# Kernel tuning notes

Hardware: AMD Instinct MI355X
Metric: run time of the kernel (lower is better)

Reference implementation:

```python
import jax, jax.numpy as jnp
import numpy as np

TARGET_MAIN_CONTRIBUTION = 0.6
CONTRIB_LOSS_COEF = 0.01
TOP_K = 2
NEG_INF = -1e9


def _gat(x, adj, W1, a1s, a1d, W2, a2s, a2d):
    """Dense 2-layer GAT (pyGAT style): multi-head concat + ELU, then one output head.
    x: [B,S,Fin], adj: [B,S,S], W1: [H,Fin,Fh], a1s/a1d: [H,Fh], W2: [H*Fh,Fout], a2s/a2d: [Fout]."""
    mask = adj > 0  # [B,S,S]
    h = jnp.einsum('bsf,hfo->bhso', x, W1)                      # [B,H,S,Fh]
    es = jnp.einsum('bhso,ho->bhs', h, a1s)
    ed = jnp.einsum('bhso,ho->bhs', h, a1d)
    e = jax.nn.leaky_relu(es[:, :, :, None] + ed[:, :, None, :], 0.2)  # [B,H,S,S]
    att = jax.nn.softmax(jnp.where(mask[:, None], e, NEG_INF), axis=-1)
    h1 = jax.nn.elu(jnp.einsum('bhst,bhto->bhso', att, h))      # [B,H,S,Fh]
    B, H, S, Fh = h1.shape
    h1 = h1.transpose(0, 2, 1, 3).reshape(B, S, H * Fh)         # concat heads
    h2 = h1 @ W2                                                # [B,S,Fout]
    e2 = jax.nn.leaky_relu((h2 @ a2s)[:, :, None] + (h2 @ a2d)[:, None, :], 0.2)
    att2 = jax.nn.softmax(jnp.where(mask, e2, NEG_INF), axis=-1)
    return jnp.einsum('bst,bto->bso', att2, h2)


def setup_inputs() -> dict:
    B, S, D, H, Hd, E = 4, 1024, 256, 6, 64, 3
    key = jax.random.key(0)
    ks = jax.random.split(key, 20)
    feature = jax.random.normal(ks[0], (B, S, D), dtype=jnp.float32)
    # sparse-ish binary adjacency with self-loops
    adj = (jax.random.uniform(ks[1], (B, S, S)) < 0.05).astype(jnp.float32)
    adj = jnp.maximum(adj, jnp.eye(S, dtype=jnp.float32)[None])
    p = lambda k, shape: jax.random.normal(k, shape, dtype=jnp.float32) * 0.1
    return {
        'feature': feature, 'adj': adj,
        'main_W1': p(ks[2], (H, D, Hd)), 'main_a1s': p(ks[3], (H, Hd)), 'main_a1d': p(ks[4], (H, Hd)),
        'main_W2': p(ks[5], (H * Hd, D)), 'main_a2s': p(ks[6], (D,)), 'main_a2d': p(ks[7], (D,)),
        'dep_W1': p(ks[8], (E, H, D, Hd)), 'dep_a1s': p(ks[9], (E, H, Hd)), 'dep_a1d': p(ks[10], (E, H, Hd)),
        'dep_W2': p(ks[11], (E, H * Hd, D)), 'dep_a2s': p(ks[12], (E, D)), 'dep_a2d': p(ks[13], (E, D)),
        'router_W': p(ks[14], (D, E)),
        'blend_W': p(ks[15], (D, D)), 'blend_b': jnp.zeros((D,), dtype=jnp.float32),
        'doc_num': 4, 'sect_num': 32,
    }


def reference(feature, adj, main_W1, main_a1s, main_a1d, main_W2, main_a2s, main_a2d,
              dep_W1, dep_a1s, dep_a1d, dep_W2, dep_a2s, dep_a2d,
              router_W, blend_W, blend_b, doc_num, sect_num):
    B, S, D = feature.shape
    E = router_W.shape[1]
    # main expert on full graph
    main_output = _gat(feature, adj, main_W1, main_a1s, main_a1d, main_W2, main_a2s, main_a2d)
    # per-expert adjacency views (zero out columns by node type)
    col = jnp.arange(S)
    sent_cols = (col < S - sect_num - doc_num).astype(adj.dtype)
    sect_cols = ((col >= S - sect_num - doc_num) & (col < S - doc_num)).astype(adj.dtype)
    doc_cols = (col >= S - doc_num).astype(adj.dtype)
    adj_stack = jnp.stack([adj * sent_cols, adj * sect_cols, adj * doc_cols])  # [E,B,S,S]
    # fixed top-k router
    x_flat = feature.reshape(-1, D)
    gate_probs = jax.nn.softmax(x_flat @ router_W, axis=-1)      # [B*S,E]
    _, top_idx = jax.lax.top_k(gate_probs, TOP_K)                # [B*S,k]
    routing_mask = jax.nn.one_hot(top_idx, E, dtype=feature.dtype).sum(axis=-2)  # [B*S,E] binary
    routing_mask = routing_mask.reshape(B, S, E)
    mask_e = routing_mask.transpose(2, 0, 1)[..., None]          # [E,B,S,1]
    # deputy experts: masked input, masked output, accumulate
    x_e = feature[None] * mask_e                                 # [E,B,S,D]
    dep_out = jax.vmap(_gat)(x_e, adj_stack, dep_W1, dep_a1s, dep_a1d, dep_W2, dep_a2s, dep_a2d)
    deputy_output = (dep_out * mask_e).sum(axis=0)               # [B,S,D]
    # blend gate
    blend_weight = jax.nn.sigmoid(feature @ blend_W + blend_b)
    final_output = blend_weight * main_output + (1.0 - blend_weight) * deputy_output
    main_contribution = blend_weight.mean()
    contribution_loss = jnp.abs(main_contribution - TARGET_MAIN_CONTRIBUTION) * CONTRIB_LOSS_COEF
    return final_output, contribution_loss, main_contribution
```

## Files before the change

### kernel.cpp

```cpp
#include <hip/hip_runtime.h>
#include <math.h>

#define B 4
#define S 1024
#define D 256
#define H 6
#define HD 64
#define NE 3
#define HHD 384
#define ROWS (B*S)
#define MAXN 128

typedef __attribute__((ext_vector_type(8))) short bf8_t;
typedef __attribute__((ext_vector_type(4))) float f32x4;

__device__ __forceinline__ float leaky(float x){ return x > 0.f ? x : 0.2f*x; }

__device__ __forceinline__ unsigned short f2bf(float f){
    union { float f; unsigned int u; } v; v.f = f;
    unsigned int u = v.u;
    return (unsigned short)((u + 0x7FFFu + ((u >> 16) & 1u)) >> 16);
}
__device__ __forceinline__ float bf2f(unsigned short h){
    union { unsigned int u; float f; } v; v.u = ((unsigned int)h) << 16;
    return v.f;
}
__device__ __forceinline__ float blo(unsigned int u){
    union { unsigned int u; float f; } v; v.u = u << 16; return v.f;
}
__device__ __forceinline__ float bhi(unsigned int u){
    union { unsigned int u; float f; } v; v.u = u & 0xffff0000u; return v.f;
}
__device__ __forceinline__ float i2f(int t){
    union { int i; float f; } v; v.i = t; return v.f;
}
__device__ __forceinline__ int f2i(float f){
    union { float f; int i; } v; v.f = f; return v.i;
}

#define PB_CONV   1024
#define PB_NBR    1024
#define PB_W1     1536
#define PB_W2     1536
#define PB_BW      256
#define PB_ZERO    177
#define PB_ROUTER 1024
#define PB_TOTAL  (PB_CONV + PB_NBR + PB_W1 + PB_W2 + PB_BW + PB_ZERO + PB_ROUTER)
#define NZERO     45088

__global__ __launch_bounds__(256) void prep_misc_kernel(
        const float* __restrict__ feature, const float* __restrict__ adj,
        const float* __restrict__ main_W1, const float* __restrict__ dep_W1,
        const float* __restrict__ main_W2, const float* __restrict__ dep_W2,
        const float* __restrict__ blend_W, const float* __restrict__ router_W,
        const int* __restrict__ doc_p, const int* __restrict__ sect_p,
        unsigned short* __restrict__ featbf, short* __restrict__ nbr,
        int4* __restrict__ nbc, unsigned short* __restrict__ w1nk,
        unsigned short* __restrict__ w2nk, unsigned short* __restrict__ bwt,
        float* __restrict__ zbase, float* __restrict__ rmask)
{
    int blk = blockIdx.x, tid = threadIdx.x;
    if (blk < PB_CONV){
        int idx = blk*256 + tid;
        float4 v = ((const float4*)feature)[idx];
        ushort4 o;
        o.x = f2bf(v.x); o.y = f2bf(v.y); o.z = f2bf(v.z); o.w = f2bf(v.w);
        ((ushort4*)featbf)[idx] = o;
        return;
    }
    blk -= PB_CONV;
    if (blk < PB_NBR){
        int wave = tid >> 6, lane = tid & 63;
        int row = blk*4 + wave;
        int b1 = S - *sect_p - *doc_p;
        int b2 = S - *doc_p;
        const float* ar = adj + (size_t)row*S + lane*16;
        float a[16];
        #pragma unroll
        for (int q = 0; q < 4; q++){
            float4 v = ((const float4*)ar)[q];
            a[q*4+0] = v.x; a[q*4+1] = v.y; a[q*4+2] = v.z; a[q*4+3] = v.w;
        }
        int t0 = lane*16;
        int k = 0, c1 = 0, c2 = 0;
        #pragma unroll
        for (int i = 0; i < 16; i++){
            if (a[i] > 0.f){
                k++;
                int t = t0 + i;
                if (t < b1) c1++;
                if (t < b2) c2++;
            }
        }
        int inc = k;
        #pragma unroll
        for (int d = 1; d < 64; d <<= 1){
            int u = __shfl_up(inc, d);
            if (lane >= d) inc += u;
        }
        int off = inc - k;
        int total = __shfl(inc, 63);
        int o = row*MAXN + off;
        #pragma unroll
        for (int i = 0; i < 16; i++){
            if (a[i] > 0.f) nbr[o++] = (short)(t0 + i);
        }
        for (int d = 32; d; d >>= 1){
            c1 += __shfl_down(c1, d);
            c2 += __shfl_down(c2, d);
        }
        if (lane == 0) nbc[row] = make_int4(total, c1, c2, 0);
        return;
    }
    blk -= PB_NBR;
    if (blk < PB_W1){
        int e = blk / 384;
        int idx = (blk - e*384)*256 + tid;
        const float* src = (e == 0) ? main_W1 : dep_W1 + (size_t)(e-1)*H*D*HD;
        int n = idx >> 8, k = idx & 255;
        int h = n >> 6, o = n & 63;
        w1nk[(size_t)e*HHD*D + idx] = f2bf(src[(h*D + k)*HD + o]);
        return;
    }
    blk -= PB_W1;
    if (blk < PB_W2){
        int g = blk*256 + tid;
        int e = g / (D*HHD);
        int rem = g - e*(D*HHD);
        int n = rem / HHD, k = rem - n*HHD;
        const float* src = (e == 0) ? main_W2 : dep_W2 + (size_t)(e-1)*HHD*D;
        w2nk[g] = f2bf(src[k*D + n]);
        return;
    }
    blk -= PB_W2;
    if (blk < PB_BW){
        int col = blk, k = tid;
        bwt[col*D + k] = f2bf(blend_W[k*D + col]);
        return;
    }
    blk -= PB_BW;
    if (blk < PB_ZERO){
        int idx = blk*256 + tid;
        if (idx < NZERO) zbase[idx] = 0.f;
        return;
    }
    blk -= PB_ZERO;
    {
        int wave = tid >> 6, lane = tid & 63;
        int row = blk*4 + wave;
        float4 xv = ((const float4*)(feature + (size_t)row*D))[lane];
        int f = lane*4;
        float xa[4] = {xv.x, xv.y, xv.z, xv.w};
        float p0 = 0.f, p1 = 0.f, p2 = 0.f;
        #pragma unroll
        for (int j = 0; j < 4; j++){
            p0 += xa[j]*router_W[(f+j)*NE + 0];
            p1 += xa[j]*router_W[(f+j)*NE + 1];
            p2 += xa[j]*router_W[(f+j)*NE + 2];
        }
        for (int off = 32; off; off >>= 1){
            p0 += __shfl_down(p0, off);
            p1 += __shfl_down(p1, off);
            p2 += __shfl_down(p2, off);
        }
        if (lane == 0){
            float p[3] = {p0, p1, p2};
            int ex = 0;
            for (int e = 1; e < NE; e++) if (p[e] <= p[ex]) ex = e;
            for (int e = 0; e < NE; e++) rmask[e*ROWS + row] = (e == ex) ? 0.f : 1.f;
        }
    }
}

__global__ __launch_bounds__(256, 4) void gemm1_kernel(const unsigned short* __restrict__ w1nk,
                                                    const unsigned short* __restrict__ featbf,
                                                    const float* __restrict__ rmask,
                                                    const float* __restrict__ main_a1s,
                                                    const float* __restrict__ main_a1d,
                                                    const float* __restrict__ dep_a1s,
                                                    const float* __restrict__ dep_a1d,
                                                    const unsigned short* __restrict__ bwt,
                                                    const float* __restrict__ bb,
                                                    unsigned short* __restrict__ htn4,
                                                    float* __restrict__ es8,
                                                    float* __restrict__ ed8,
                                                    float* __restrict__ meanV1p,
                                                    float* __restrict__ gatebuf,
                                                    float* __restrict__ sumBuf){
    __shared__ float ep[2][2][64][17];
    int tid = threadIdx.x, wave = tid >> 6, lane = tid & 63;
    int quad = lane >> 4, l16 = lane & 15;
    int e = blockIdx.z;
    int n0 = blockIdx.y*64;
    f32x4 z4 = {0.f,0.f,0.f,0.f};
    bf8_t bz = {0,0,0,0,0,0,0,0};

    if (e == 4){
        if (blockIdx.x >= 2) return;
        int m0 = blockIdx.x*128;
        const unsigned short* arow0 = bwt + (size_t)(m0 + wave*16 + l16)*D + quad*8;
        const unsigned short* arow1 = arow0 + (size_t)64*D;
        const unsigned short* brow[4];
        #pragma unroll
        for (int j = 0; j < 4; j++)
            brow[j] = featbf + (size_t)(n0 + j*16 + l16)*D + quad*8;
        f32x4 acc[8] = {z4, z4, z4, z4, z4, z4, z4, z4};
        bf8_t a0F = *(const bf8_t*)(arow0);
        bf8_t a1F = *(const bf8_t*)(arow1);
        bf8_t bF[4];
        #pragma unroll
        for (int j = 0; j < 4; j++) bF[j] = *(const bf8_t*)(brow[j]);
        #pragma unroll
        for (int it = 0; it < D/32; it++){
            bf8_t a0C = a0F, a1C = a1F;
            bf8_t bC[4] = {bF[0], bF[1], bF[2], bF[3]};
            if (it + 1 < D/32){
                int kn = (it + 1)*32;
                a0F = *(const bf8_t*)(arow0 + kn);
                a1F = *(const bf8_t*)(arow1 + kn);
                #pragma unroll
                for (int j = 0; j < 4; j++) bF[j] = *(const bf8_t*)(brow[j] + kn);
            }
            #pragma unroll
            for (int j = 0; j < 4; j++){
                acc[j]   = __builtin_amdgcn_mfma_f32_16x16x32_bf16(a0C, bC[j], acc[j],   0, 0, 0);
                acc[4+j] = __builtin_amdgcn_mfma_f32_16x16x32_bf16(a1C, bC[j], acc[4+j], 0, 0, 0);
            }
        }
        int mbase0 = m0 + wave*16 + quad*4;
        int mbase1 = mbase0 + 64;
        float bias0[4], bias1[4];
        #pragma unroll
        for (int r = 0; r < 4; r++){ bias0[r] = bb[mbase0 + r]; bias1[r] = bb[mbase1 + r]; }
        float lsum = 0.f;
        #pragma unroll
        for (int j = 0; j < 4; j++){
            int rown = n0 + j*16 + l16;
            f32x4 st0, st1;
            #pragma unroll
            for (int r = 0; r < 4; r++){
                float g0 = 1.f/(1.f + __expf(-(acc[j][r] + bias0[r])));
                float g1 = 1.f/(1.f + __expf(-(acc[4+j][r] + bias1[r])));
                lsum += g0 + g1;
                st0[r] = g0; st1[r] = g1;
            }
            *(f32x4*)(gatebuf + (size_t)rown*D + mbase0) = st0;
            *(f32x4*)(gatebuf + (size_t)rown*D + mbase1) = st1;
        }
        float* redp = &ep[0][0][0][0];
        redp[tid] = lsum;
        __syncthreads();
        for (int sft = 128; sft; sft >>= 1){
            if (tid < sft) redp[tid] += redp[tid + sft];
            __syncthreads();
        }
        if (tid == 0) atomicAdd(sumBuf, redp[0]);
        return;
    }

    int p = blockIdx.x;
    int m0 = p*128;
    const unsigned short* arow0 = w1nk + (size_t)e*HHD*D + (size_t)(m0 + wave*16 + l16)*D + quad*8;
    const unsigned short* arow1 = arow0 + (size_t)64*D;
    const unsigned short* brow[4];
    bool zr[4];
    #pragma unroll
    for (int j = 0; j < 4; j++){
        int n = n0 + j*16 + l16;
        brow[j] = featbf + (size_t)n*D + quad*8;
        zr[j] = (e > 0) ? (rmask[(size_t)(e-1)*ROWS + n] == 0.f) : false;
    }
    f32x4 acc[8] = {z4, z4, z4, z4, z4, z4, z4, z4};
    bf8_t a0F = *(const bf8_t*)(arow0);
    bf8_t a1F = *(const bf8_t*)(arow1);
    bf8_t bF[4];
    #pragma unroll
    for (int j = 0; j < 4; j++) bF[j] = zr[j] ? bz : *(const bf8_t*)(brow[j]);
    #pragma unroll
    for (int it = 0; it < D/32; it++){
        bf8_t a0C = a0F, a1C = a1F;
        bf8_t bC[4] = {bF[0], bF[1], bF[2], bF[3]};
        if (it + 1 < D/32){
            int kn = (it + 1)*32;
            a0F = *(const bf8_t*)(arow0 + kn);
            a1F = *(const bf8_t*)(arow1 + kn);
            #pragma unroll
            for (int j = 0; j < 4; j++) bF[j] = zr[j] ? bz : *(const bf8_t*)(brow[j] + kn);
        }
        #pragma unroll
        for (int j = 0; j < 4; j++){
            acc[j]   = __builtin_amdgcn_mfma_f32_16x16x32_bf16(a0C, bC[j], acc[j],   0, 0, 0);
            acc[4+j] = __builtin_amdgcn_mfma_f32_16x16x32_bf16(a1C, bC[j], acc[4+j], 0, 0, 0);
        }
    }
    int b = n0 >> 10;
    int mbase0 = m0 + wave*16 + quad*4;
    int mbase1 = mbase0 + 64;
    int obase = wave*16 + quad*4;
    int h0 = p*2, h1 = p*2 + 1;
    #pragma unroll
    for (int j = 0; j < 4; j++){
        int row = n0 + j*16 + l16;
        ushort4 o0, o1;
        o0.x = f2bf(acc[j][0]);   o0.y = f2bf(acc[j][1]);
        o0.z = f2bf(acc[j][2]);   o0.w = f2bf(acc[j][3]);
        o1.x = f2bf(acc[4+j][0]); o1.y = f2bf(acc[4+j][1]);
        o1.z = f2bf(acc[4+j][2]); o1.w = f2bf(acc[4+j][3]);
        *(ushort4*)(htn4 + ((size_t)e*ROWS + row)*HHD + mbase0) = o0;
        *(ushort4*)(htn4 + ((size_t)e*ROWS + row)*HHD + mbase1) = o1;
    }
    const float* a1sp = (e == 0) ? main_a1s : dep_a1s + (size_t)(e-1)*H*HD;
    const float* a1dp = (e == 0) ? main_a1d : dep_a1d + (size_t)(e-1)*H*HD;
    float s0v[4], d0v[4], s1v[4], d1v[4];
    #pragma unroll
    for (int r = 0; r < 4; r++){
        s0v[r] = a1sp[mbase0 + r]; d0v[r] = a1dp[mbase0 + r];
        s1v[r] = a1sp[mbase1 + r]; d1v[r] = a1dp[mbase1 + r];
    }
    #pragma unroll
    for (int j = 0; j < 4; j++){
        float ps0 = 0.f, pd0 = 0.f, ps1 = 0.f, pd1 = 0.f;
        #pragma unroll
        for (int r = 0; r < 4; r++){
            ps0 += acc[j][r]*s0v[r];   pd0 += acc[j][r]*d0v[r];
            ps1 += acc[4+j][r]*s1v[r]; pd1 += acc[4+j][r]*d1v[r];
        }
        ep[0][0][j*16 + l16][wave*4 + quad] = ps0;
        ep[0][1][j*16 + l16][wave*4 + quad] = pd0;
        ep[1][0][j*16 + l16][wave*4 + quad] = ps1;
        ep[1][1][j*16 + l16][wave*4 + quad] = pd1;
    }
    float* mvb = meanV1p + ((size_t)e*B + b)*512;
    #pragma unroll
    for (int r = 0; r < 4; r++){
        float cm0 = acc[0][r] + acc[1][r] + acc[2][r] + acc[3][r];
        float cm1 = acc[4][r] + acc[5][r] + acc[6][r] + acc[7][r];
        for (int off = 8; off; off >>= 1){
            cm0 += __shfl_down(cm0, off, 16);
            cm1 += __shfl_down(cm1, off, 16);
        }
        if (l16 == 0){
            atomicAdd(mvb + (obase + r)*8 + h0, cm0*(1.f/(float)S));
            atomicAdd(mvb + (obase + r)*8 + h1, cm1*(1.f/(float)S));
        }
    }
    __syncthreads();
    {
        int hh = tid >> 7, arr = (tid >> 6) & 1, sl = tid & 63;
        float sum = 0.f;
        #pragma unroll
        for (int i = 0; i < 16; i++) sum += ep[hh][arr][sl][i];
        int n = n0 + sl;
        float* dst = arr ? ed8 : es8;
        dst[(((size_t)e*B + (n >> 10))*S + (n & 1023))*8 + (p*2 + hh)] = sum;
    }
}

__global__ __launch_bounds__(128) void attn1_gather_kernel(const unsigned short* __restrict__ htn4,
                                                           const float* __restrict__ es8,
                                                           const float* __restrict__ ed8,
                                                           const short* __restrict__ nbr,
                                                           const int4* __restrict__ nbc,
                                                           const float* __restrict__ meanV1p,
                                                           unsigned short* __restrict__ h1c4){
    __shared__ float wrec[MAXN][8];
    __shared__ float pacc[64][8];
    __shared__ float pden[2][8];
    int wave = threadIdx.x >> 6, lane = threadIdx.x & 63;
    int s = blockIdx.x;
    int e = blockIdx.y >> 2, b = blockIdx.y & 3;
    int row = b*S + s;
    int4 c = nbc[row];
    int lo = 0, hi = c.x;
    if (e == 1) hi = c.y;
    else if (e == 2){ lo = c.y; hi = c.z; }
    else if (e == 3){ lo = c.z; }
    int nn = hi - lo;
    const float* esp = es8 + (((size_t)e*B + b)*S + s)*8;
    f32x4 es_lo = *(const f32x4*)esp;
    f32x4 es_hi = *(const f32x4*)(esp + 4);
    float esv[6] = {es_lo[0], es_lo[1], es_lo[2], es_lo[3], es_hi[0], es_hi[1]};
    const float* edb = ed8 + ((size_t)e*B + b)*S*8;
    const short* nl = nbr + (size_t)row*MAXN;
    int i = wave*64 + lane;
    float w[6] = {0,0,0,0,0,0};
    if (i < nn){
        int t = nl[lo + i];
        const float* epn = edb + (size_t)t*8;
        f32x4 d0 = *(const f32x4*)epn;
        f32x4 d1 = *(const f32x4*)(epn + 4);
        float edv[6] = {d0[0], d0[1], d0[2], d0[3], d1[0], d1[1]};
        #pragma unroll
        for (int h = 0; h < 6; h++) w[h] = __expf(leaky(esv[h] + edv[h]));
        f32x4 r0 = {w[0], w[1], w[2], w[3]};
        f32x4 r1 = {w[4], w[5], i2f(t), 0.f};
        *(f32x4*)&wrec[i][0] = r0;
        *(f32x4*)&wrec[i][4] = r1;
    }
    #pragma unroll
    for (int h = 0; h < 6; h++){
        float x = w[h];
        for (int o2 = 32; o2; o2 >>= 1) x += __shfl_down(x, o2);
        if (lane == 0) pden[wave][h] = x;
    }
    __syncthreads();
    const unsigned short* Vb = htn4 + ((size_t)e*ROWS + b*S)*HHD + lane;
    float acc[6] = {0,0,0,0,0,0};
    #pragma unroll 4
    for (int j = wave; j < nn; j += 2){
        f32x4 r0 = *(const f32x4*)&wrec[j][0];
        f32x4 r1 = *(const f32x4*)&wrec[j][4];
        int t = f2i(r1[2]);
        const unsigned short* vp = Vb + (size_t)t*HHD;
        float v0 = bf2f(vp[0]);
        float v1 = bf2f(vp[64]);
        float v2 = bf2f(vp[128]);
        float v3 = bf2f(vp[192]);
        float v4 = bf2f(vp[256]);
        float v5 = bf2f(vp[320]);
        acc[0] += r0[0]*v0; acc[1] += r0[1]*v1;
        acc[2] += r0[2]*v2; acc[3] += r0[3]*v3;
        acc[4] += r1[0]*v4; acc[5] += r1[1]*v5;
    }
    if (wave == 1){
        f32x4 p0 = {acc[0], acc[1], acc[2], acc[3]};
        f32x4 p1 = {acc[4], acc[5], 0.f, 0.f};
        *(f32x4*)&pacc[lane][0] = p0;
        *(f32x4*)&pacc[lane][4] = p1;
    }
    __syncthreads();
    if (wave == 0){
        unsigned short* outp = h1c4 + ((size_t)e*ROWS + row)*HHD;
        const float* mv = meanV1p + ((size_t)e*B + b)*512 + lane*8;
        #pragma unroll
        for (int h = 0; h < 6; h++){
            float den = pden[0][h] + pden[1][h];
            float v = (nn > 0) ? (acc[h] + pacc[lane][h])/den : mv[h];
            v = v > 0.f ? v : __expf(v) - 1.f;
            outp[h*64 + lane] = f2bf(v);
        }
    }
}

__global__ __launch_bounds__(256, 4) void gemm2_kernel(const unsigned short* __restrict__ w2nk,
                                                    const unsigned short* __restrict__ h1c4,
                                                    const float* __restrict__ main_a2s,
                                                    const float* __restrict__ main_a2d,
                                                    const float* __restrict__ dep_a2s,
                                                    const float* __restrict__ dep_a2d,
                                                    unsigned short* __restrict__ h2n4,
                                                    float* __restrict__ f2s4,
                                                    float* __restrict__ f2d4,
                                                    float* __restrict__ meanV2){
    __shared__ float ep[2][2][64][17];
    int tid = threadIdx.x, wave = tid >> 6, lane = tid & 63;
    int quad = lane >> 4, l16 = lane & 15;
    int e = blockIdx.z;
    int m0 = blockIdx.x*128;
    int n0 = blockIdx.y*64;
    f32x4 z4 = {0.f,0.f,0.f,0.f};
    const unsigned short* arow0 = w2nk + (size_t)e*D*HHD + (size_t)(m0 + wave*16 + l16)*HHD + quad*8;
    const unsigned short* arow1 = arow0 + (size_t)64*HHD;
    const unsigned short* brow[4];
    #pragma unroll
    for (int j = 0; j < 4; j++)
        brow[j] = h1c4 + (size_t)e*ROWS*HHD + (size_t)(n0 + j*16 + l16)*HHD + quad*8;
    f32x4 acc[8] = {z4, z4, z4, z4, z4, z4, z4, z4};
    bf8_t a0F = *(const bf8_t*)(arow0);
    bf8_t a1F = *(const bf8_t*)(arow1);
    bf8_t bF[4];
    #pragma unroll
    for (int j = 0; j < 4; j++) bF[j] = *(const bf8_t*)(brow[j]);
    #pragma unroll
    for (int it = 0; it < HHD/32; it++){
        bf8_t a0C = a0F, a1C = a1F;
        bf8_t bC[4] = {bF[0], bF[1], bF[2], bF[3]};
        if (it + 1 < HHD/32){
            int kn = (it + 1)*32;
            a0F = *(const bf8_t*)(arow0 + kn);
            a1F = *(const bf8_t*)(arow1 + kn);
            #pragma unroll
            for (int j = 0; j < 4; j++) bF[j] = *(const bf8_t*)(brow[j] + kn);
        }
        #pragma unroll
        for (int j = 0; j < 4; j++){
            acc[j]   = __builtin_amdgcn_mfma_f32_16x16x32_bf16(a0C, bC[j], acc[j],   0, 0, 0);
            acc[4+j] = __builtin_amdgcn_mfma_f32_16x16x32_bf16(a1C, bC[j], acc[4+j], 0, 0, 0);
        }
    }
    int b = n0 >> 10;
    int mbase0 = m0 + wave*16 + quad*4;
    int mbase1 = mbase0 + 64;
    #pragma unroll
    for (int j = 0; j < 4; j++){
        int row = n0 + j*16 + l16;
        ushort4 o0, o1;
        o0.x = f2bf(acc[j][0]);   o0.y = f2bf(acc[j][1]);
        o0.z = f2bf(acc[j][2]);   o0.w = f2bf(acc[j][3]);
        o1.x = f2bf(acc[4+j][0]); o1.y = f2bf(acc[4+j][1]);
        o1.z = f2bf(acc[4+j][2]); o1.w = f2bf(acc[4+j][3]);
        *(ushort4*)(h2n4 + ((size_t)e*ROWS + row)*D + mbase0) = o0;
        *(ushort4*)(h2n4 + ((size_t)e*ROWS + row)*D + mbase1) = o1;
    }
    const float* a2sp = (e == 0) ? main_a2s : dep_a2s + (size_t)(e-1)*D;
    const float* a2dp = (e == 0) ? main_a2d : dep_a2d + (size_t)(e-1)*D;
    float s0v[4], d0v[4], s1v[4], d1v[4];
    #pragma unroll
    for (int r = 0; r < 4; r++){
        s0v[r] = a2sp[mbase0 + r]; d0v[r] = a2dp[mbase0 + r];
        s1v[r] = a2sp[mbase1 + r]; d1v[r] = a2dp[mbase1 + r];
    }
    #pragma unroll
    for (int j = 0; j < 4; j++){
        float ps0 = 0.f, pd0 = 0.f, ps1 = 0.f, pd1 = 0.f;
        #pragma unroll
        for (int r = 0; r < 4; r++){
            ps0 += acc[j][r]*s0v[r];   pd0 += acc[j][r]*d0v[r];
            ps1 += acc[4+j][r]*s1v[r]; pd1 += acc[4+j][r]*d1v[r];
        }
        ep[0][0][j*16 + l16][wave*4 + quad] = ps0;
        ep[0][1][j*16 + l16][wave*4 + quad] = pd0;
        ep[1][0][j*16 + l16][wave*4 + quad] = ps1;
        ep[1][1][j*16 + l16][wave*4 + quad] = pd1;
    }
    #pragma unroll
    for (int r = 0; r < 4; r++){
        float cm0 = acc[0][r] + acc[1][r] + acc[2][r] + acc[3][r];
        float cm1 = acc[4][r] + acc[5][r] + acc[6][r] + acc[7][r];
        for (int off = 8; off; off >>= 1){
            cm0 += __shfl_down(cm0, off, 16);
            cm1 += __shfl_down(cm1, off, 16);
        }
        if (l16 == 0){
            atomicAdd(meanV2 + ((size_t)e*B + b)*D + mbase0 + r, cm0*(1.f/(float)S));
            atomicAdd(meanV2 + ((size_t)e*B + b)*D + mbase1 + r, cm1*(1.f/(float)S));
        }
    }
    __syncthreads();
    {
        int hh = tid >> 7, arr = (tid >> 6) & 1, sl = tid & 63;
        float sum = 0.f;
        #pragma unroll
        for (int i = 0; i < 16; i++) sum += ep[hh][arr][sl][i];
        int n = n0 + sl;
        float* dst = arr ? f2d4 : f2s4;
        atomicAdd(dst + (size_t)e*ROWS + n, sum);
    }
}

__global__ __launch_bounds__(256) void attn2_blend_kernel(const unsigned short* __restrict__ h2n4,
                                                          const float* __restrict__ f2s4,
                                                          const float* __restrict__ f2d4,
                                                          const short* __restrict__ nbr,
                                                          const int4* __restrict__ nbc,
                                                          const float* __restrict__ meanV2,
                                                          const float* __restrict__ gatebuf,
                                                          const float* __restrict__ rmask,
                                                          const float* __restrict__ sumBuf,
                                                          float* __restrict__ outp){
    __shared__ float2 wrec0[MAXN];
    __shared__ float2 wrec1[MAXN];
    __shared__ float pacc[3][256];
    __shared__ float pden[4][4];
    int wave = threadIdx.x >> 6, lane = threadIdx.x & 63;
    int s = blockIdx.x, b = blockIdx.y;
    int row = b*S + s;
    int4 c = nbc[row];
    float rm0 = rmask[row], rm1 = rmask[ROWS + row], rm2 = rmask[2*ROWS + row];
    const short* nl = nbr + (size_t)row*MAXN;
    if (wave < 2){
        int i = wave*64 + lane;
        float w = 0.f;
        if (i < c.x){
            int t = nl[i];
            float fs = f2s4[row];
            w = __expf(leaky(fs + f2d4[(size_t)b*S + t]));
            float2 r; r.x = w; r.y = i2f(t);
            wrec0[i] = r;
        }
        float dsum = w;
        for (int o2 = 32; o2; o2 >>= 1) dsum += __shfl_down(dsum, o2);
        if (lane == 0) pden[wave][0] = dsum;
    } else {
        int i = (wave - 2)*64 + lane;
        float w = 0.f, d1 = 0.f, d2 = 0.f, d3 = 0.f;
        if (i < c.x){
            int t = nl[i];
            int tag = (i < c.y) ? 1 : ((i < c.z) ? 2 : 3);
            float act = (tag == 1) ? rm0 : ((tag == 2) ? rm1 : rm2);
            if (act != 0.f){
                float fs = f2s4[(size_t)tag*ROWS + row];
                w = __expf(leaky(fs + f2d4[(size_t)tag*ROWS + (size_t)b*S + t]));
            }
            float2 r; r.x = w; r.y = i2f(t);
            wrec1[i] = r;
            if (tag == 1) d1 = w; else if (tag == 2) d2 = w; else d3 = w;
        }
        for (int o2 = 32; o2; o2 >>= 1){
            d1 += __shfl_down(d1, o2);
            d2 += __shfl_down(d2, o2);
            d3 += __shfl_down(d3, o2);
        }
        if (lane == 0){ pden[wave][1] = d1; pden[wave][2] = d2; pden[wave][3] = d3; }
    }
    __syncthreads();
    float acc[4] = {0.f, 0.f, 0.f, 0.f};
    if (wave < 2){
        float inv = 1.f/(pden[0][0] + pden[1][0]);
        const unsigned short* V = h2n4 + (size_t)b*S*D;
        #pragma unroll 4
        for (int j = wave; j < c.x; j += 2){
            float2 r = wrec0[j];
            float wv = r.x*inv;
            int t = f2i(r.y);
            const unsigned short* vp = V + (size_t)t*D + lane*4;
            uint2 dv = *(const uint2*)vp;
            acc[0] += wv*blo(dv.x); acc[1] += wv*bhi(dv.x);
            acc[2] += wv*blo(dv.y); acc[3] += wv*bhi(dv.y);
        }
    } else {
        int rlo[3] = {0, c.y, c.z};
        int rhi[3] = {c.y, c.z, c.x};
        float ract[3] = {rm0, rm1, rm2};
        for (int rg = 0; rg < 3; rg++){
            if (ract[rg] == 0.f || rhi[rg] <= rlo[rg]) continue;
            float inv = 1.f/(pden[2][rg+1] + pden[3][rg+1]);
            const unsigned short* V = h2n4 + ((size_t)(rg+1)*ROWS + (size_t)b*S)*D;
            #pragma unroll 4
            for (int j = rlo[rg] + (wave - 2); j < rhi[rg]; j += 2){
                float2 r = wrec1[j];
                float wv = r.x*inv;
                int t = f2i(r.y);
                const unsigned short* vp = V + (size_t)t*D + lane*4;
                uint2 dv = *(const uint2*)vp;
                acc[0] += wv*blo(dv.x); acc[1] += wv*bhi(dv.x);
                acc[2] += wv*blo(dv.y); acc[3] += wv*bhi(dv.y);
            }
        }
    }
    if (wave >= 1){
        #pragma unroll
        for (int q = 0; q < 4; q++) pacc[wave-1][lane*4 + q] = acc[q];
    }
    __syncthreads();
    if (wave == 0){
        float4 g4 = *(const float4*)(gatebuf + (size_t)row*D + lane*4);
        float dep_mv[4] = {0.f, 0.f, 0.f, 0.f};
        if (rm0 != 0.f && c.y == 0){
            float4 mv = *(const float4*)(meanV2 + ((size_t)1*B + b)*D + lane*4);
            dep_mv[0] += mv.x; dep_mv[1] += mv.y; dep_mv[2] += mv.z; dep_mv[3] += mv.w;
        }
        if (rm1 != 0.f && c.z == c.y){
            float4 mv = *(const float4*)(meanV2 + ((size_t)2*B + b)*D + lane*4);
            dep_mv[0] += mv.x; dep_mv[1] += mv.y; dep_mv[2] += mv.z; dep_mv[3] += mv.w;
        }
        if (rm2 != 0.f && c.x == c.z){
            float4 mv = *(const float4*)(meanV2 + ((size_t)3*B + b)*D + lane*4);
            dep_mv[0] += mv.x; dep_mv[1] += mv.y; dep_mv[2] += mv.z; dep_mv[3] += mv.w;
        }
        float g[4] = {g4.x, g4.y, g4.z, g4.w};
        float4 o;
        float* op = &o.x;
        #pragma unroll
        for (int q = 0; q < 4; q++){
            int col = lane*4 + q;
            float a0 = acc[q] + pacc[0][col];
            float dep = pacc[1][col] + pacc[2][col] + dep_mv[q];
            op[q] = g[q]*a0 + (1.f - g[q])*dep;
        }
        *(float4*)(outp + (size_t)row*D + lane*4) = o;
    }
    if (blockIdx.x == 0 && blockIdx.y == 0 && threadIdx.x == 0){
        float mc = sumBuf[0] / (float)(ROWS*D);
        outp[ROWS*D]     = fabsf(mc - 0.6f)*0.01f;
        outp[ROWS*D + 1] = mc;
    }
}

extern "C" void kernel_launch(void* const* d_in, const int* in_sizes, int n_in,
                              void* d_out, int out_size, void* d_ws, size_t ws_size,
                              hipStream_t stream)
{
    const float* feature  = (const float*)d_in[0];
    const float* adj      = (const float*)d_in[1];
    const float* main_W1  = (const float*)d_in[2];
    const float* main_a1s = (const float*)d_in[3];
    const float* main_a1d = (const float*)d_in[4];
    const float* main_W2  = (const float*)d_in[5];
    const float* main_a2s = (const float*)d_in[6];
    const float* main_a2d = (const float*)d_in[7];
    const float* dep_W1   = (const float*)d_in[8];
    const float* dep_a1s  = (const float*)d_in[9];
    const float* dep_a1d  = (const float*)d_in[10];
    const float* dep_W2   = (const float*)d_in[11];
    const float* dep_a2s  = (const float*)d_in[12];
    const float* dep_a2d  = (const float*)d_in[13];
    const float* router_W = (const float*)d_in[14];
    const float* blend_W  = (const float*)d_in[15];
    const float* blend_b  = (const float*)d_in[16];
    const int*   doc_p    = (const int*)d_in[17];
    const int*   sect_p   = (const int*)d_in[18];

    char* ws = (char*)d_ws;
    size_t off = 0;
    unsigned short* featbf = (unsigned short*)(ws + off); off += (size_t)ROWS*D*2;
    short*          nbr    = (short*)(ws + off);          off += (size_t)ROWS*MAXN*2;
    int4*           nbc    = (int4*)(ws + off);           off += (size_t)ROWS*16;
    unsigned short* w1nk   = (unsigned short*)(ws + off); off += (size_t)4*HHD*D*2;
    unsigned short* w2nk   = (unsigned short*)(ws + off); off += (size_t)4*D*HHD*2;
    unsigned short* bwt    = (unsigned short*)(ws + off); off += (size_t)D*D*2;
    float* es8 = (float*)(ws + off); off += (size_t)4*B*S*8*4;
    float* ed8 = (float*)(ws + off); off += (size_t)4*B*S*8*4;
    float* gatebuf = (float*)(ws + off); off += (size_t)ROWS*D*4;
    unsigned short* htn4 = (unsigned short*)(ws + off); off += (size_t)4*ROWS*HHD*2;
    unsigned short* h2n4 = (unsigned short*)(ws + off); off += (size_t)4*ROWS*D*2;
    unsigned short* h1c4 = (unsigned short*)(ws + off); off += (size_t)4*ROWS*HHD*2;
    float* f2s4    = (float*)(ws + off); off += (size_t)4*ROWS*4;
    float* f2d4    = (float*)(ws + off); off += (size_t)4*ROWS*4;
    float* meanV1p = (float*)(ws + off); off += (size_t)4*B*512*4;
    float* meanV2  = (float*)(ws + off); off += (size_t)4*B*D*4;
    float* sumBuf  = (float*)(ws + off); off += 128;
    float* rmask   = (float*)(ws + off); off += (size_t)NE*ROWS*4;
    float* outp    = (float*)d_out;

    prep_misc_kernel<<<PB_TOTAL, 256, 0, stream>>>(
        feature, adj, main_W1, dep_W1, main_W2, dep_W2, blend_W, router_W,
        doc_p, sect_p, featbf, nbr, nbc, w1nk, w2nk, bwt, f2s4, rmask);

    gemm1_kernel<<<dim3(3, ROWS/64, 5), 256, 0, stream>>>(w1nk, featbf, rmask,
        main_a1s, main_a1d, dep_a1s, dep_a1d, bwt, blend_b,
        htn4, es8, ed8, meanV1p, gatebuf, sumBuf);
    attn1_gather_kernel<<<dim3(S, 16), 128, 0, stream>>>(htn4, es8, ed8, nbr, nbc,
        meanV1p, h1c4);
    gemm2_kernel<<<dim3(D/128, ROWS/64, 4), 256, 0, stream>>>(w2nk, h1c4,
        main_a2s, main_a2d, dep_a2s, dep_a2d, h2n4, f2s4, f2d4, meanV2);
    attn2_blend_kernel<<<dim3(S, B), 256, 0, stream>>>(h2n4, f2s4, f2d4, nbr, nbc,
        meanV2, gatebuf, rmask, sumBuf, outp);
}
```

Before: 212.3 us.

## Fuse five stage kernels into one persistent cooperative kernel with grid syncs

Turns each stage kernel into a device task function and runs all stages inside one cooperative persistent kernel with 1024 blocks, using grid-wide syncs between stages in place of separate kernel launches. If the cooperative launch fails, it falls back to five separate launches. The aim is to remove launch overhead and the gaps between kernels. In exchange it fixes the occupancy to 1024 blocks at 256 threads, caps registers at four blocks per CU, forces shared memory to the largest stage's size, and adds grid-barrier cost. Stages with many small tasks, such as attention1 with 16384 tasks, now loop inside fewer blocks.

```diff
diff --git a/kernel.cpp b/kernel.cpp
--- a/kernel.cpp
+++ b/kernel.cpp
@@ -1,5 +1,8 @@
 #include <hip/hip_runtime.h>
+#include <hip/hip_cooperative_groups.h>
 #include <math.h>
+
+namespace cg = cooperative_groups;
 
 #define B 4
 #define S 1024
@@ -10,6 +13,7 @@
 #define HHD 384
 #define ROWS (B*S)
 #define MAXN 128
+#define NBLK 1024
 
 typedef __attribute__((ext_vector_type(8))) short bf8_t;
 typedef __attribute__((ext_vector_type(4))) float f32x4;
@@ -37,6 +41,21 @@
 __device__ __forceinline__ int f2i(float f){
     union { float f; int i; } v; v.f = f; return v.i;
 }
+
+struct P {
+    const float *feature, *adj;
+    const float *main_W1, *dep_W1, *main_W2, *dep_W2, *blend_W, *router_W;
+    const int *doc_p, *sect_p;
+    const float *main_a1s, *main_a1d, *dep_a1s, *dep_a1d;
+    const float *main_a2s, *main_a2d, *dep_a2s, *dep_a2d;
+    const float *blend_b;
+    unsigned short *featbf; short *nbr; int4 *nbc;
+    unsigned short *w1nk, *w2nk, *bwt;
+    float *es8, *ed8, *gatebuf;
+    unsigned short *htn4, *h2n4, *h1c4;
+    float *f2s4, *f2d4, *meanV1p, *meanV2, *sumBuf, *rmask;
+    float *outp;
+};
 
 #define PB_CONV   1024
 #define PB_NBR    1024
@@ -48,33 +67,24 @@
 #define PB_TOTAL  (PB_CONV + PB_NBR + PB_W1 + PB_W2 + PB_BW + PB_ZERO + PB_ROUTER)
 #define NZERO     45088
 
-__global__ __launch_bounds__(256) void prep_misc_kernel(
-        const float* __restrict__ feature, const float* __restrict__ adj,
-        const float* __restrict__ main_W1, const float* __restrict__ dep_W1,
-        const float* __restrict__ main_W2, const float* __restrict__ dep_W2,
-        const float* __restrict__ blend_W, const float* __restrict__ router_W,
-        const int* __restrict__ doc_p, const int* __restrict__ sect_p,
-        unsigned short* __restrict__ featbf, short* __restrict__ nbr,
-        int4* __restrict__ nbc, unsigned short* __restrict__ w1nk,
-        unsigned short* __restrict__ w2nk, unsigned short* __restrict__ bwt,
-        float* __restrict__ zbase, float* __restrict__ rmask)
+__device__ __forceinline__ void prep_task(const P& pp, int task, int tid)
 {
-    int blk = blockIdx.x, tid = threadIdx.x;
+    int blk = task;
     if (blk < PB_CONV){
         int idx = blk*256 + tid;
-        float4 v = ((const float4*)feature)[idx];
+        float4 v = ((const float4*)pp.feature)[idx];
         ushort4 o;
         o.x = f2bf(v.x); o.y = f2bf(v.y); o.z = f2bf(v.z); o.w = f2bf(v.w);
-        ((ushort4*)featbf)[idx] = o;
+        ((ushort4*)pp.featbf)[idx] = o;
         return;
     }
     blk -= PB_CONV;
     if (blk < PB_NBR){
         int wave = tid >> 6, lane = tid & 63;
         int row = blk*4 + wave;
-        int b1 = S - *sect_p - *doc_p;
-        int b2 = S - *doc_p;
-        const float* ar = adj + (size_t)row*S + lane*16;
+        int b1 = S - *pp.sect_p - *pp.doc_p;
+        int b2 = S - *pp.doc_p;
+        const float* ar = pp.adj + (size_t)row*S + lane*16;
         float a[16];
         #pragma unroll
         for (int q = 0; q < 4; q++){
@@ -103,23 +113,23 @@
         int o = row*MAXN + off;
         #pragma unroll
         for (int i = 0; i < 16; i++){
-            if (a[i] > 0.f) nbr[o++] = (short)(t0 + i);
+            if (a[i] > 0.f) pp.nbr[o++] = (short)(t0 + i);
         }
         for (int d = 32; d; d >>= 1){
             c1 += __shfl_down(c1, d);
             c2 += __shfl_down(c2, d);
         }
-        if (lane == 0) nbc[row] = make_int4(total, c1, c2, 0);
+        if (lane == 0) pp.nbc[row] = make_int4(total, c1, c2, 0);
         return;
     }
     blk -= PB_NBR;
     if (blk < PB_W1){
         int e = blk / 384;
         int idx = (blk - e*384)*256 + tid;
-        const float* src = (e == 0) ? main_W1 : dep_W1 + (size_t)(e-1)*H*D*HD;
+        const float* src = (e == 0) ? pp.main_W1 : pp.dep_W1 + (size_t)(e-1)*H*D*HD;
         int n = idx >> 8, k = idx & 255;
         int h = n >> 6, o = n & 63;
-        w1nk[(size_t)e*HHD*D + idx] = f2bf(src[(h*D + k)*HD + o]);
+        pp.w1nk[(size_t)e*HHD*D + idx] = f2bf(src[(h*D + k)*HD + o]);
         return;
     }
     blk -= PB_W1;
@@ -128,35 +138,35 @@
         int e = g / (D*HHD);
         int rem = g - e*(D*HHD);
         int n = rem / HHD, k = rem - n*HHD;
-        const float* src = (e == 0) ? main_W2 : dep_W2 + (size_t)(e-1)*HHD*D;
-        w2nk[g] = f2bf(src[k*D + n]);
+        const float* src = (e == 0) ? pp.main_W2 : pp.dep_W2 + (size_t)(e-1)*HHD*D;
+        pp.w2nk[g] = f2bf(src[k*D + n]);
         return;
     }
     blk -= PB_W2;
     if (blk < PB_BW){
         int col = blk, k = tid;
-        bwt[col*D + k] = f2bf(blend_W[k*D + col]);
+        pp.bwt[col*D + k] = f2bf(pp.blend_W[k*D + col]);
         return;
     }
     blk -= PB_BW;
     if (blk < PB_ZERO){
         int idx = blk*256 + tid;
-        if (idx < NZERO) zbase[idx] = 0.f;
+        if (idx < NZERO) pp.f2s4[idx] = 0.f;
         return;
     }
     blk -= PB_ZERO;
     {
         int wave = tid >> 6, lane = tid & 63;
         int row = blk*4 + wave;
-        float4 xv = ((const float4*)(feature + (size_t)row*D))[lane];
+        float4 xv = ((const float4*)(pp.feature + (size_t)row*D))[lane];
         int f = lane*4;
         float xa[4] = {xv.x, xv.y, xv.z, xv.w};
         float p0 = 0.f, p1 = 0.f, p2 = 0.f;
         #pragma unroll
         for (int j = 0; j < 4; j++){
-            p0 += xa[j]*router_W[(f+j)*NE + 0];
-            p1 += xa[j]*router_W[(f+j)*NE + 1];
-            p2 += xa[j]*router_W[(f+j)*NE + 2];
+            p0 += xa[j]*pp.router_W[(f+j)*NE + 0];
+            p1 += xa[j]*pp.router_W[(f+j)*NE + 1];
+            p2 += xa[j]*pp.router_W[(f+j)*NE + 2];
         }
         for (int off = 32; off; off >>= 1){
             p0 += __shfl_down(p0, off);
@@ -167,43 +177,29 @@
             float p[3] = {p0, p1, p2};
             int ex = 0;
             for (int e = 1; e < NE; e++) if (p[e] <= p[ex]) ex = e;
-            for (int e = 0; e < NE; e++) rmask[e*ROWS + row] = (e == ex) ? 0.f : 1.f;
-        }
-    }
-}
-
-__global__ __launch_bounds__(256, 4) void gemm1_kernel(const unsigned short* __restrict__ w1nk,
-                                                    const unsigned short* __restrict__ featbf,
-                                                    const float* __restrict__ rmask,
-                                                    const float* __restrict__ main_a1s,
-                                                    const float* __restrict__ main_a1d,
-                                                    const float* __restrict__ dep_a1s,
-                                                    const float* __restrict__ dep_a1d,
-                                                    const unsigned short* __restrict__ bwt,
-                                                    const float* __restrict__ bb,
-                                                    unsigned short* __restrict__ htn4,
-                                                    float* __restrict__ es8,
-                                                    float* __restrict__ ed8,
-                                                    float* __restrict__ meanV1p,
-                                                    float* __restrict__ gatebuf,
-                                                    float* __restrict__ sumBuf){
-    __shared__ float ep[2][2][64][17];
-    int tid = threadIdx.x, wave = tid >> 6, lane = tid & 63;
+            for (int e = 0; e < NE; e++) pp.rmask[e*ROWS + row] = (e == ex) ? 0.f : 1.f;
+        }
+    }
+}
+
+__device__ __forceinline__ void g1_task(const P& pp, int task, int tid, float* smem)
+{
+    float (*ep)[2][64][17] = (float (*)[2][64][17])smem;
+    int wave = tid >> 6, lane = tid & 63;
     int quad = lane >> 4, l16 = lane & 15;
-    int e = blockIdx.z;
-    int n0 = blockIdx.y*64;
     f32x4 z4 = {0.f,0.f,0.f,0.f};
     bf8_t bz = {0,0,0,0,0,0,0,0};
 
-    if (e == 4){
-        if (blockIdx.x >= 2) return;
-        int m0 = blockIdx.x*128;
-        const unsigned short* arow0 = bwt + (size_t)(m0 + wave*16 + l16)*D + quad*8;
+    if (task >= 768){
+        int g = task - 768;
+        int m0 = (g >> 6)*128;
+        int n0 = (g & 63)*64;
+        const unsigned short* arow0 = pp.bwt + (size_t)(m0 + wave*16 + l16)*D + quad*8;
         const unsigned short* arow1 = arow0 + (size_t)64*D;
         const unsigned short* brow[4];
         #pragma unroll
         for (int j = 0; j < 4; j++)
-            brow[j] = featbf + (size_t)(n0 + j*16 + l16)*D + quad*8;
+            brow[j] = pp.featbf + (size_t)(n0 + j*16 + l16)*D + quad*8;
         f32x4 acc[8] = {z4, z4, z4, z4, z4, z4, z4, z4};
         bf8_t a0F = *(const bf8_t*)(arow0);
         bf8_t a1F = *(const bf8_t*)(arow1);
@@ -231,7 +227,7 @@
         int mbase1 = mbase0 + 64;
         float bias0[4], bias1[4];
         #pragma unroll
-        for (int r = 0; r < 4; r++){ bias0[r] = bb[mbase0 + r]; bias1[r] = bb[mbase1 + r]; }
+        for (int r = 0; r < 4; r++){ bias0[r] = pp.blend_b[mbase0 + r]; bias1[r] = pp.blend_b[mbase1 + r]; }
         float lsum = 0.f;
         #pragma unroll
         for (int j = 0; j < 4; j++){
@@ -244,172 +240,176 @@
                 lsum += g0 + g1;
                 st0[r] = g0; st1[r] = g1;
             }
-            *(f32x4*)(gatebuf + (size_t)rown*D + mbase0) = st0;
-            *(f32x4*)(gatebuf + (size_t)rown*D + mbase1) = st1;
-        }
-        float* redp = &ep[0][0][0][0];
+            *(f32x4*)(pp.gatebuf + (size_t)rown*D + mbase0) = st0;
+            *(f32x4*)(pp.gatebuf + (size_t)rown*D + mbase1) = st1;
+        }
+        float* redp = smem;
         redp[tid] = lsum;
         __syncthreads();
         for (int sft = 128; sft; sft >>= 1){
             if (tid < sft) redp[tid] += redp[tid + sft];
             __syncthreads();
         }
-        if (tid == 0) atomicAdd(sumBuf, redp[0]);
-        return;
-    }
-
-    int p = blockIdx.x;
-    int m0 = p*128;
-    const unsigned short* arow0 = w1nk + (size_t)e*HHD*D + (size_t)(m0 + wave*16 + l16)*D + quad*8;
-    const unsigned short* arow1 = arow0 + (size_t)64*D;
-    const unsigned short* brow[4];
-    bool zr[4];
-    #pragma unroll
-    for (int j = 0; j < 4; j++){
-        int n = n0 + j*16 + l16;
-        brow[j] = featbf + (size_t)n*D + quad*8;
-        zr[j] = (e > 0) ? (rmask[(size_t)(e-1)*ROWS + n] == 0.f) : false;
-    }
-    f32x4 acc[8] = {z4, z4, z4, z4, z4, z4, z4, z4};
-    bf8_t a0F = *(const bf8_t*)(arow0);
-    bf8_t a1F = *(const bf8_t*)(arow1);
-    bf8_t bF[4];
-    #pragma unroll
-    for (int j = 0; j < 4; j++) bF[j] = zr[j] ? bz : *(const bf8_t*)(brow[j]);
-    #pragma unroll
-    for (int it = 0; it < D/32; it++){
-        bf8_t a0C = a0F, a1C = a1F;
-        bf8_t bC[4] = {bF[0], bF[1], bF[2], bF[3]};
-        if (it + 1 < D/32){
-            int kn = (it + 1)*32;
-            a0F = *(const bf8_t*)(arow0 + kn);
-            a1F = *(const bf8_t*)(arow1 + kn);
+        if (tid == 0) atomicAdd(pp.sumBuf, redp[0]);
+    } else {
+        int e = task / 192;
+        int rem = task - e*192;
+        int p = rem >> 6;
+        int n0 = (rem & 63)*64;
+        int m0 = p*128;
+        const unsigned short* arow0 = pp.w1nk + (size_t)e*HHD*D + (size_t)(m0 + wave*16 + l16)*D + quad*8;
+        const unsigned short* arow1 = arow0 + (size_t)64*D;
+        const unsigned short* brow[4];
+        bool zr[4];
+        #pragma unroll
+        for (int j = 0; j < 4; j++){
+            int n = n0 + j*16 + l16;
+            brow[j] = pp.featbf + (size_t)n*D + quad*8;
+            zr[j] = (e > 0) ? (pp.rmask[(size_t)(e-1)*ROWS + n] == 0.f) : false;
+        }
+        f32x4 acc[8] = {z4, z4, z4, z4, z4, z4, z4, z4};
+        bf8_t a0F = *(const bf8_t*)(arow0);
+        bf8_t a1F = *(const bf8_t*)(arow1);
+        bf8_t bF[4];
+        #pragma unroll
+        for (int j = 0; j < 4; j++) bF[j] = zr[j] ? bz : *(const bf8_t*)(brow[j]);
+        #pragma unroll
+        for (int it = 0; it < D/32; it++){
+            bf8_t a0C = a0F, a1C = a1F;
+            bf8_t bC[4] = {bF[0], bF[1], bF[2], bF[3]};
+            if (it + 1 < D/32){
+                int kn = (it + 1)*32;
+                a0F = *(const bf8_t*)(arow0 + kn);
+                a1F = *(const bf8_t*)(arow1 + kn);
+                #pragma unroll
+                for (int j = 0; j < 4; j++) bF[j] = zr[j] ? bz : *(const bf8_t*)(brow[j] + kn);
+            }
             #pragma unroll
-            for (int j = 0; j < 4; j++) bF[j] = zr[j] ? bz : *(const bf8_t*)(brow[j] + kn);
-        }
+            for (int j = 0; j < 4; j++){
+                acc[j]   = __builtin_amdgcn_mfma_f32_16x16x32_bf16(a0C, bC[j], acc[j],   0, 0, 0);
+                acc[4+j] = __builtin_amdgcn_mfma_f32_16x16x32_bf16(a1C, bC[j], acc[4+j], 0, 0, 0);
+            }
+        }
+        int b = n0 >> 10;
+        int mbase0 = m0 + wave*16 + quad*4;
+        int mbase1 = mbase0 + 64;
+        int obase = wave*16 + quad*4;
+        int h0 = p*2, h1 = p*2 + 1;
         #pragma unroll
         for (int j = 0; j < 4; j++){
-            acc[j]   = __builtin_amdgcn_mfma_f32_16x16x32_bf16(a0C, bC[j], acc[j],   0, 0, 0);
-            acc[4+j] = __builtin_amdgcn_mfma_f32_16x16x32_bf16(a1C, bC[j], acc[4+j], 0, 0, 0);
-        }
-    }
-    int b = n0 >> 10;
-    int mbase0 = m0 + wave*16 + quad*4;
-    int mbase1 = mbase0 + 64;
-    int obase = wave*16 + quad*4;
-    int h0 = p*2, h1 = p*2 + 1;
-    #pragma unroll
-    for (int j = 0; j < 4; j++){
-        int row = n0 + j*16 + l16;
-        ushort4 o0, o1;
-        o0.x = f2bf(acc[j][0]);   o0.y = f2bf(acc[j][1]);
-        o0.z = f2bf(acc[j][2]);   o0.w = f2bf(acc[j][3]);
-        o1.x = f2bf(acc[4+j][0]); o1.y = f2bf(acc[4+j][1]);
-        o1.z = f2bf(acc[4+j][2]); o1.w = f2bf(acc[4+j][3]);
-        *(ushort4*)(htn4 + ((size_t)e*ROWS + row)*HHD + mbase0) = o0;
-        *(ushort4*)(htn4 + ((size_t)e*ROWS + row)*HHD + mbase1) = o1;
-    }
-    const float* a1sp = (e == 0) ? main_a1s : dep_a1s + (size_t)(e-1)*H*HD;
-    const float* a1dp = (e == 0) ? main_a1d : dep_a1d + (size_t)(e-1)*H*HD;
-    float s0v[4], d0v[4], s1v[4], d1v[4];
-    #pragma unroll
-    for (int r = 0; r < 4; r++){
-        s0v[r] = a1sp[mbase0 + r]; d0v[r] = a1dp[mbase0 + r];
-        s1v[r] = a1sp[mbase1 + r]; d1v[r] = a1dp[mbase1 + r];
-    }
-    #pragma unroll
-    for (int j = 0; j < 4; j++){
-        float ps0 = 0.f, pd0 = 0.f, ps1 = 0.f, pd1 = 0.f;
+            int row = n0 + j*16 + l16;
+            ushort4 o0, o1;
+            o0.x = f2bf(acc[j][0]);   o0.y = f2bf(acc[j][1]);
+            o0.z = f2bf(acc[j][2]);   o0.w = f2bf(acc[j][3]);
+            o1.x = f2bf(acc[4+j][0]); o1.y = f2bf(acc[4+j][1]);
+            o1.z = f2bf(acc[4+j][2]); o1.w = f2bf(acc[4+j][3]);
+            *(ushort4*)(pp.htn4 + ((size_t)e*ROWS + row)*HHD + mbase0) = o0;
+            *(ushort4*)(pp.htn4 + ((size_t)e*ROWS + row)*HHD + mbase1) = o1;
+        }
+        const float* a1sp = (e == 0) ? pp.main_a1s : pp.dep_a1s + (size_t)(e-1)*H*HD;
+        const float* a1dp = (e == 0) ? pp.main_a1d : pp.dep_a1d + (size_t)(e-1)*H*HD;
+        float s0v[4], d0v[4], s1v[4], d1v[4];
         #pragma unroll
         for (int r = 0; r < 4; r++){
-            ps0 += acc[j][r]*s0v[r];   pd0 += acc[j][r]*d0v[r];
-            ps1 += acc[4+j][r]*s1v[r]; pd1 += acc[4+j][r]*d1v[r];
-        }
-        ep[0][0][j*16 + l16][wave*4 + quad] = ps0;
-        ep[0][1][j*16 + l16][wave*4 + quad] = pd0;
-        ep[1][0][j*16 + l16][wave*4 + quad] = ps1;
-        ep[1][1][j*16 + l16][wave*4 + quad] = pd1;
-    }
-    float* mvb = meanV1p + ((size_t)e*B + b)*512;
-    #pragma unroll
-    for (int r = 0; r < 4; r++){
-        float cm0 = acc[0][r] + acc[1][r] + acc[2][r] + acc[3][r];
-        float cm1 = acc[4][r] + acc[5][r] + acc[6][r] + acc[7][r];
-        for (int off = 8; off; off >>= 1){
-            cm0 += __shfl_down(cm0, off, 16);
-            cm1 += __shfl_down(cm1, off, 16);
-        }
-        if (l16 == 0){
-            atomicAdd(mvb + (obase + r)*8 + h0, cm0*(1.f/(float)S));
-            atomicAdd(mvb + (obase + r)*8 + h1, cm1*(1.f/(float)S));
-        }
-    }
-    __syncthreads();
-    {
-        int hh = tid >> 7, arr = (tid >> 6) & 1, sl = tid & 63;
-        float sum = 0.f;
-        #pragma unroll
-        for (int i = 0; i < 16; i++) sum += ep[hh][arr][sl][i];
-        int n = n0 + sl;
-        float* dst = arr ? ed8 : es8;
-        dst[(((size_t)e*B + (n >> 10))*S + (n & 1023))*8 + (p*2 + hh)] = sum;
-    }
-}
-
-__global__ __launch_bounds__(128) void attn1_gather_kernel(const unsigned short* __restrict__ htn4,
-                                                           const float* __restrict__ es8,
-                                                           const float* __restrict__ ed8,
-                                                           const short* __restrict__ nbr,
-                                                           const int4* __restrict__ nbc,
-                                                           const float* __restrict__ meanV1p,
-                                                           unsigned short* __restrict__ h1c4){
-    __shared__ float wrec[MAXN][8];
-    __shared__ float pacc[64][8];
-    __shared__ float pden[2][8];
-    int wave = threadIdx.x >> 6, lane = threadIdx.x & 63;
-    int s = blockIdx.x;
-    int e = blockIdx.y >> 2, b = blockIdx.y & 3;
+            s0v[r] = a1sp[mbase0 + r]; d0v[r] = a1dp[mbase0 + r];
+            s1v[r] = a1sp[mbase1 + r]; d1v[r] = a1dp[mbase1 + r];
+        }
+        #pragma unroll
+        for (int j = 0; j < 4; j++){
+            float ps0 = 0.f, pd0 = 0.f, ps1 = 0.f, pd1 = 0.f;
+            #pragma unroll
+            for (int r = 0; r < 4; r++){
+                ps0 += acc[j][r]*s0v[r];   pd0 += acc[j][r]*d0v[r];
+                ps1 += acc[4+j][r]*s1v[r]; pd1 += acc[4+j][r]*d1v[r];
+            }
+            ep[0][0][j*16 + l16][wave*4 + quad] = ps0;
+            ep[0][1][j*16 + l16][wave*4 + quad] = pd0;
+            ep[1][0][j*16 + l16][wave*4 + quad] = ps1;
+            ep[1][1][j*16 + l16][wave*4 + quad] = pd1;
+        }
+        float* mvb = pp.meanV1p + ((size_t)e*B + b)*512;
+        #pragma unroll
+        for (int r = 0; r < 4; r++){
+            float cm0 = acc[0][r] + acc[1][r] + acc[2][r] + acc[3][r];
+            float cm1 = acc[4][r] + acc[5][r] + acc[6][r] + acc[7][r];
+            for (int off = 8; off; off >>= 1){
+                cm0 += __shfl_down(cm0, off, 16);
+                cm1 += __shfl_down(cm1, off, 16);
+            }
+            if (l16 == 0){
+                atomicAdd(mvb + (obase + r)*8 + h0, cm0*(1.f/(float)S));
+                atomicAdd(mvb + (obase + r)*8 + h1, cm1*(1.f/(float)S));
+            }
+        }
+        __syncthreads();
+        {
+            int hh = tid >> 7, arr = (tid >> 6) & 1, sl = tid & 63;
+            float sum = 0.f;
+            #pragma unroll
+            for (int i = 0; i < 16; i++) sum += ep[hh][arr][sl][i];
+            int n = n0 + sl;
+            float* dst = arr ? pp.ed8 : pp.es8;
+            dst[(((size_t)e*B + (n >> 10))*S + (n & 1023))*8 + (p*2 + hh)] = sum;
+        }
+    }
+    __syncthreads();
+}
+
+__device__ __forceinline__ void a1_task(const P& pp, int task, int tid, float* smem)
+{
+    float* wrec = smem;
+    float* pacc = smem + 1024;
+    float* pden = smem + 2560;
+    int wave = tid >> 6, lane = tid & 63;
+    int eb = task >> 10;
+    int s = task & 1023;
+    int e = eb >> 2, b = eb & 3;
     int row = b*S + s;
-    int4 c = nbc[row];
+    int4 c = pp.nbc[row];
     int lo = 0, hi = c.x;
     if (e == 1) hi = c.y;
     else if (e == 2){ lo = c.y; hi = c.z; }
     else if (e == 3){ lo = c.z; }
     int nn = hi - lo;
-    const float* esp = es8 + (((size_t)e*B + b)*S + s)*8;
-    f32x4 es_lo = *(const f32x4*)esp;
-    f32x4 es_hi = *(const f32x4*)(esp + 4);
-    float esv[6] = {es_lo[0], es_lo[1], es_lo[2], es_lo[3], es_hi[0], es_hi[1]};
-    const float* edb = ed8 + ((size_t)e*B + b)*S*8;
-    const short* nl = nbr + (size_t)row*MAXN;
-    int i = wave*64 + lane;
-    float w[6] = {0,0,0,0,0,0};
-    if (i < nn){
-        int t = nl[lo + i];
-        const float* epn = edb + (size_t)t*8;
-        f32x4 d0 = *(const f32x4*)epn;
-        f32x4 d1 = *(const f32x4*)(epn + 4);
-        float edv[6] = {d0[0], d0[1], d0[2], d0[3], d1[0], d1[1]};
-        #pragma unroll
-        for (int h = 0; h < 6; h++) w[h] = __expf(leaky(esv[h] + edv[h]));
-        f32x4 r0 = {w[0], w[1], w[2], w[3]};
-        f32x4 r1 = {w[4], w[5], i2f(t), 0.f};
-        *(f32x4*)&wrec[i][0] = r0;
-        *(f32x4*)&wrec[i][4] = r1;
-    }
-    #pragma unroll
-    for (int h = 0; h < 6; h++){
-        float x = w[h];
-        for (int o2 = 32; o2; o2 >>= 1) x += __shfl_down(x, o2);
-        if (lane == 0) pden[wave][h] = x;
-    }
-    __syncthreads();
-    const unsigned short* Vb = htn4 + ((size_t)e*ROWS + b*S)*HHD + lane;
+    const short* nl = pp.nbr + (size_t)row*MAXN;
+    if (wave < 2){
+        const float* esp = pp.es8 + (((size_t)e*B + b)*S + s)*8;
+        f32x4 es_lo = *(const f32x4*)esp;
+        f32x4 es_hi = *(const f32x4*)(esp + 4);
+        float esv[6] = {es_lo[0], es_lo[1], es_lo[2], es_lo[3], es_hi[0], es_hi[1]};
+        const float* edb = pp.ed8 + ((size_t)e*B + b)*S*8;
+        int i = wave*64 + lane;
+        float w[6] = {0,0,0,0,0,0};
+        if (i < nn){
+            int t = nl[lo + i];
+            const float* epn = edb + (size_t)t*8;
+            f32x4 d0 = *(const f32x4*)epn;
+            f32x4 d1 = *(const f32x4*)(epn + 4);
+            float edv[6] = {d0[0], d0[1], d0[2], d0[3], d1[0], d1[1]};
+            #pragma unroll
+            for (int h = 0; h < 6; h++) w[h] = __expf(leaky(esv[h] + edv[h]));
+            float zf = 0.f;
+            if (e > 0 && pp.rmask[(size_t)(e-1)*ROWS + (size_t)b*S + t] == 0.f) zf = 1.f;
+            f32x4 r0 = {w[0], w[1], w[2], w[3]};
+            f32x4 r1 = {w[4], w[5], i2f(t), zf};
+            *(f32x4*)&wrec[i*8]     = r0;
+            *(f32x4*)&wrec[i*8 + 4] = r1;
+        }
+        #pragma unroll
+        for (int h = 0; h < 6; h++){
+            float x = w[h];
+            for (int o2 = 32; o2; o2 >>= 1) x += __shfl_down(x, o2);
+            if (lane == 0) pden[wave*8 + h] = x;
+        }
+    }
+    __syncthreads();
+    const unsigned short* Vb = pp.htn4 + ((size_t)e*ROWS + b*S)*HHD + lane;
     float acc[6] = {0,0,0,0,0,0};
-    #pragma unroll 4
-    for (int j = wave; j < nn; j += 2){
-        f32x4 r0 = *(const f32x4*)&wrec[j][0];
-        f32x4 r1 = *(const f32x4*)&wrec[j][4];
+    #pragma unroll 2
+    for (int j = wave; j < nn; j += 4){
+        f32x4 r0 = *(const f32x4*)&wrec[j*8];
+        f32x4 r1 = *(const f32x4*)&wrec[j*8 + 4];
+        if (r1[3] != 0.f) continue;
         int t = f2i(r1[2]);
         const unsigned short* vp = Vb + (size_t)t*HHD;
         float v0 = bf2f(vp[0]);
@@ -422,49 +422,45 @@
         acc[2] += r0[2]*v2; acc[3] += r0[3]*v3;
         acc[4] += r1[0]*v4; acc[5] += r1[1]*v5;
     }
-    if (wave == 1){
+    if (wave >= 1){
+        float* pb = pacc + (size_t)(wave-1)*512 + lane*8;
         f32x4 p0 = {acc[0], acc[1], acc[2], acc[3]};
         f32x4 p1 = {acc[4], acc[5], 0.f, 0.f};
-        *(f32x4*)&pacc[lane][0] = p0;
-        *(f32x4*)&pacc[lane][4] = p1;
+        *(f32x4*)pb = p0;
+        *(f32x4*)(pb + 4) = p1;
     }
     __syncthreads();
     if (wave == 0){
-        unsigned short* outp = h1c4 + ((size_t)e*ROWS + row)*HHD;
-        const float* mv = meanV1p + ((size_t)e*B + b)*512 + lane*8;
+        unsigned short* outp = pp.h1c4 + ((size_t)e*ROWS + row)*HHD;
+        const float* mv = pp.meanV1p + ((size_t)e*B + b)*512 + lane*8;
         #pragma unroll
         for (int h = 0; h < 6; h++){
-            float den = pden[0][h] + pden[1][h];
-            float v = (nn > 0) ? (acc[h] + pacc[lane][h])/den : mv[h];
+            float den = pden[h] + pden[8 + h];
+            float v = (nn > 0) ? (acc[h] + pacc[lane*8 + h] + pacc[512 + lane*8 + h] + pacc[1024 + lane*8 + h])/den
+                               : mv[h];
             v = v > 0.f ? v : __expf(v) - 1.f;
             outp[h*64 + lane] = f2bf(v);
         }
     }
-}
-
-__global__ __launch_bounds__(256, 4) void gemm2_kernel(const unsigned short* __restrict__ w2nk,
-                                                    const unsigned short* __restrict__ h1c4,
-                                                    const float* __restrict__ main_a2s,
-                                                    const float* __restrict__ main_a2d,
-                                                    const float* __restrict__ dep_a2s,
-                                                    const float* __restrict__ dep_a2d,
-                                                    unsigned short* __restrict__ h2n4,
-                                                    float* __restrict__ f2s4,
-                                                    float* __restrict__ f2d4,
-                                                    float* __restrict__ meanV2){
-    __shared__ float ep[2][2][64][17];
-    int tid = threadIdx.x, wave = tid >> 6, lane = tid & 63;
+    __syncthreads();
+}
+
+__device__ __forceinline__ void g2_task(const P& pp, int task, int tid, float* smem)
+{
+    float (*ep)[2][64][17] = (float (*)[2][64][17])smem;
+    int wave = tid >> 6, lane = tid & 63;
     int quad = lane >> 4, l16 = lane & 15;
-    int e = blockIdx.z;
-    int m0 = blockIdx.x*128;
-    int n0 = blockIdx.y*64;
+    int e = task >> 7;
+    int rem = task & 127;
+    int m0 = (rem >> 6)*128;
+    int n0 = (rem & 63)*64;
     f32x4 z4 = {0.f,0.f,0.f,0.f};
-    const unsigned short* arow0 = w2nk + (size_t)e*D*HHD + (size_t)(m0 + wave*16 + l16)*HHD + quad*8;
+    const unsigned short* arow0 = pp.w2nk + (size_t)e*D*HHD + (size_t)(m0 + wave*16 + l16)*HHD + quad*8;
     const unsigned short* arow1 = arow0 + (size_t)64*HHD;
     const unsigned short* brow[4];
     #pragma unroll
     for (int j = 0; j < 4; j++)
-        brow[j] = h1c4 + (size_t)e*ROWS*HHD + (size_t)(n0 + j*16 + l16)*HHD + quad*8;
+        brow[j] = pp.h1c4 + (size_t)e*ROWS*HHD + (size_t)(n0 + j*16 + l16)*HHD + quad*8;
     f32x4 acc[8] = {z4, z4, z4, z4, z4, z4, z4, z4};
     bf8_t a0F = *(const bf8_t*)(arow0);
     bf8_t a1F = *(const bf8_t*)(arow1);
@@ -499,11 +495,11 @@
         o0.z = f2bf(acc[j][2]);   o0.w = f2bf(acc[j][3]);
         o1.x = f2bf(acc[4+j][0]); o1.y = f2bf(acc[4+j][1]);
         o1.z = f2bf(acc[4+j][2]); o1.w = f2bf(acc[4+j][3]);
-        *(ushort4*)(h2n4 + ((size_t)e*ROWS + row)*D + mbase0) = o0;
-        *(ushort4*)(h2n4 + ((size_t)e*ROWS + row)*D + mbase1) = o1;
-    }
-    const float* a2sp = (e == 0) ? main_a2s : dep_a2s + (size_t)(e-1)*D;
-    const float* a2dp = (e == 0) ? main_a2d : dep_a2d + (size_t)(e-1)*D;
+        *(ushort4*)(pp.h2n4 + ((size_t)e*ROWS + row)*D + mbase0) = o0;
+        *(ushort4*)(pp.h2n4 + ((size_t)e*ROWS + row)*D + mbase1) = o1;
+    }
+    const float* a2sp = (e == 0) ? pp.main_a2s : pp.dep_a2s + (size_t)(e-1)*D;
+    const float* a2dp = (e == 0) ? pp.main_a2d : pp.dep_a2d + (size_t)(e-1)*D;
     float s0v[4], d0v[4], s1v[4], d1v[4];
     #pragma unroll
     for (int r = 0; r < 4; r++){
@@ -532,8 +528,8 @@
             cm1 += __shfl_down(cm1, off, 16);
         }
         if (l16 == 0){
-            atomicAdd(meanV2 + ((size_t)e*B + b)*D + mbase0 + r, cm0*(1.f/(float)S));
-            atomicAdd(meanV2 + ((size_t)e*B + b)*D + mbase1 + r, cm1*(1.f/(float)S));
+            atomicAdd(pp.meanV2 + ((size_t)e*B + b)*D + mbase0 + r, cm0*(1.f/(float)S));
+            atomicAdd(pp.meanV2 + ((size_t)e*B + b)*D + mbase1 + r, cm1*(1.f/(float)S));
         }
     }
     __syncthreads();
@@ -543,44 +539,37 @@
         #pragma unroll
         for (int i = 0; i < 16; i++) sum += ep[hh][arr][sl][i];
         int n = n0 + sl;
-        float* dst = arr ? f2d4 : f2s4;
+        float* dst = arr ? pp.f2d4 : pp.f2s4;
         atomicAdd(dst + (size_t)e*ROWS + n, sum);
     }
-}
-
-__global__ __launch_bounds__(256) void attn2_blend_kernel(const unsigned short* __restrict__ h2n4,
-                                                          const float* __restrict__ f2s4,
-                                                          const float* __restrict__ f2d4,
-                                                          const short* __restrict__ nbr,
-                                                          const int4* __restrict__ nbc,
-                                                          const float* __restrict__ meanV2,
-                                                          const float* __restrict__ gatebuf,
-                                                          const float* __restrict__ rmask,
-                                                          const float* __restrict__ sumBuf,
-                                                          float* __restrict__ outp){
-    __shared__ float2 wrec0[MAXN];
-    __shared__ float2 wrec1[MAXN];
-    __shared__ float pacc[3][256];
-    __shared__ float pden[4][4];
-    int wave = threadIdx.x >> 6, lane = threadIdx.x & 63;
-    int s = blockIdx.x, b = blockIdx.y;
+    __syncthreads();
+}
+
+__device__ __forceinline__ void a2_task(const P& pp, int task, int tid, float* smem)
+{
+    float2* wrec0 = (float2*)smem;
+    float2* wrec1 = (float2*)(smem + 256);
+    float*  pacc  = smem + 512;
+    float*  pden  = smem + 1280;
+    int wave = tid >> 6, lane = tid & 63;
+    int b = task >> 10, s = task & 1023;
     int row = b*S + s;
-    int4 c = nbc[row];
-    float rm0 = rmask[row], rm1 = rmask[ROWS + row], rm2 = rmask[2*ROWS + row];
-    const short* nl = nbr + (size_t)row*MAXN;
+    int4 c = pp.nbc[row];
+    float rm0 = pp.rmask[row], rm1 = pp.rmask[ROWS + row], rm2 = pp.rmask[2*ROWS + row];
+    const short* nl = pp.nbr + (size_t)row*MAXN;
     if (wave < 2){
         int i = wave*64 + lane;
         float w = 0.f;
         if (i < c.x){
             int t = nl[i];
-            float fs = f2s4[row];
-            w = __expf(leaky(fs + f2d4[(size_t)b*S + t]));
+            float fs = pp.f2s4[row];
+            w = __expf(leaky(fs + pp.f2d4[(size_t)b*S + t]));
             float2 r; r.x = w; r.y = i2f(t);
             wrec0[i] = r;
         }
         float dsum = w;
         for (int o2 = 32; o2; o2 >>= 1) dsum += __shfl_down(dsum, o2);
-        if (lane == 0) pden[wave][0] = dsum;
+        if (lane == 0) pden[wave*4 + 0] = dsum;
     } else {
         int i = (wave - 2)*64 + lane;
         float w = 0.f, d1 = 0.f, d2 = 0.f, d3 = 0.f;
@@ -589,8 +578,8 @@
             int tag = (i < c.y) ? 1 : ((i < c.z) ? 2 : 3);
             float act = (tag == 1) ? rm0 : ((tag == 2) ? rm1 : rm2);
             if (act != 0.f){
-                float fs = f2s4[(size_t)tag*ROWS + row];
-                w = __expf(leaky(fs + f2d4[(size_t)tag*ROWS + (size_t)b*S + t]));
+                float fs = pp.f2s4[(size_t)tag*ROWS + row];
+                w = __expf(leaky(fs + pp.f2d4[(size_t)tag*ROWS + (size_t)b*S + t]));
             }
             float2 r; r.x = w; r.y = i2f(t);
             wrec1[i] = r;
@@ -601,13 +590,13 @@
             d2 += __shfl_down(d2, o2);
             d3 += __shfl_down(d3, o2);
         }
-        if (lane == 0){ pden[wave][1] = d1; pden[wave][2] = d2; pden[wave][3] = d3; }
+        if (lane == 0){ pden[wave*4 + 1] = d1; pden[wave*4 + 2] = d2; pden[wave*4 + 3] = d3; }
     }
     __syncthreads();
     float acc[4] = {0.f, 0.f, 0.f, 0.f};
     if (wave < 2){
-        float inv = 1.f/(pden[0][0] + pden[1][0]);
-        const unsigned short* V = h2n4 + (size_t)b*S*D;
+        float inv = 1.f/(pden[0] + pden[4]);
+        const unsigned short* V = pp.h2n4 + (size_t)b*S*D;
         #pragma unroll 4
         for (int j = wave; j < c.x; j += 2){
             float2 r = wrec0[j];
@@ -624,8 +613,8 @@
         float ract[3] = {rm0, rm1, rm2};
         for (int rg = 0; rg < 3; rg++){
             if (ract[rg] == 0.f || rhi[rg] <= rlo[rg]) continue;
-            float inv = 1.f/(pden[2][rg+1] + pden[3][rg+1]);
-            const unsigned short* V = h2n4 + ((size_t)(rg+1)*ROWS + (size_t)b*S)*D;
+            float inv = 1.f/(pden[2*4 + rg + 1] + pden[3*4 + rg + 1]);
+            const unsigned short* V = pp.h2n4 + ((size_t)(rg+1)*ROWS + (size_t)b*S)*D;
             #pragma unroll 4
             for (int j = rlo[rg] + (wave - 2); j < rhi[rg]; j += 2){
                 float2 r = wrec1[j];
@@ -640,22 +629,22 @@
     }
     if (wave >= 1){
         #pragma unroll
-        for (int q = 0; q < 4; q++) pacc[wave-1][lane*4 + q] = acc[q];
+        for (int q = 0; q < 4; q++) pacc[(size_t)(wave-1)*256 + lane*4 + q] = acc[q];
     }
     __syncthreads();
     if (wave == 0){
-        float4 g4 = *(const float4*)(gatebuf + (size_t)row*D + lane*4);
+        float4 g4 = *(const float4*)(pp.gatebuf + (size_t)row*D + lane*4);
         float dep_mv[4] = {0.f, 0.f, 0.f, 0.f};
         if (rm0 != 0.f && c.y == 0){
-            float4 mv = *(const float4*)(meanV2 + ((size_t)1*B + b)*D + lane*4);
+            float4 mv = *(const float4*)(pp.meanV2 + ((size_t)1*B + b)*D + lane*4);
             dep_mv[0] += mv.x; dep_mv[1] += mv.y; dep_mv[2] += mv.z; dep_mv[3] += mv.w;
         }
         if (rm1 != 0.f && c.z == c.y){
-            float4 mv = *(const float4*)(meanV2 + ((size_t)2*B + b)*D + lane*4);
+            float4 mv = *(const float4*)(pp.meanV2 + ((size_t)2*B + b)*D + lane*4);
             dep_mv[0] += mv.x; dep_mv[1] += mv.y; dep_mv[2] += mv.z; dep_mv[3] += mv.w;
         }
         if (rm2 != 0.f && c.x == c.z){
-            float4 mv = *(const float4*)(meanV2 + ((size_t)3*B + b)*D + lane*4);
+            float4 mv = *(const float4*)(pp.meanV2 + ((size_t)3*B + b)*D + lane*4);
             dep_mv[0] += mv.x; dep_mv[1] += mv.y; dep_mv[2] += mv.z; dep_mv[3] += mv.w;
         }
         float g[4] = {g4.x, g4.y, g4.z, g4.w};
@@ -664,76 +653,110 @@
         #pragma unroll
         for (int q = 0; q < 4; q++){
             int col = lane*4 + q;
-            float a0 = acc[q] + pacc[0][col];
-            float dep = pacc[1][col] + pacc[2][col] + dep_mv[q];
+            float a0 = acc[q] + pacc[col];
+            float dep = pacc[256 + col] + pacc[512 + col] + dep_mv[q];
             op[q] = g[q]*a0 + (1.f - g[q])*dep;
         }
-        *(float4*)(outp + (size_t)row*D + lane*4) = o;
-    }
-    if (blockIdx.x == 0 && blockIdx.y == 0 && threadIdx.x == 0){
-        float mc = sumBuf[0] / (float)(ROWS*D);
-        outp[ROWS*D]     = fabsf(mc - 0.6f)*0.01f;
-        outp[ROWS*D + 1] = mc;
-    }
+        *(float4*)(pp.outp + (size_t)row*D + lane*4) = o;
+    }
+    if (task == 0 && tid == 0){
+        float mc = pp.sumBuf[0] / (float)(ROWS*D);
+        pp.outp[ROWS*D]     = fabsf(mc - 0.6f)*0.01f;
+        pp.outp[ROWS*D + 1] = mc;
+    }
+    __syncthreads();
+}
+
+__global__ __launch_bounds__(256, 4) void fused_kernel(P pp)
+{
+    __shared__ __align__(16) float smem[4352];
+    cg::grid_group gg = cg::this_grid();
+    int tid = threadIdx.x;
+    for (int t = blockIdx.x; t < PB_TOTAL; t += NBLK) prep_task(pp, t, tid);
+    gg.sync();
+    for (int t = blockIdx.x; t < 896; t += NBLK) g1_task(pp, t, tid, smem);
+    gg.sync();
+    for (int t = blockIdx.x; t < 16384; t += NBLK) a1_task(pp, t, tid, smem);
+    gg.sync();
+    for (int t = blockIdx.x; t < 512; t += NBLK) g2_task(pp, t, tid, smem);
+    gg.sync();
+    for (int t = blockIdx.x; t < 4096; t += NBLK) a2_task(pp, t, tid, smem);
+}
+
+__global__ __launch_bounds__(256) void prep_sk(P pp){ prep_task(pp, blockIdx.x, threadIdx.x); }
+__global__ __launch_bounds__(256, 4) void g1_sk(P pp){
+    __shared__ __align__(16) float smem[4352];
+    g1_task(pp, blockIdx.x, threadIdx.x, smem);
+}
+__global__ __launch_bounds__(256) void a1_sk(P pp){
+    __shared__ __align__(16) float smem[2576];
+    a1_task(pp, blockIdx.x, threadIdx.x, smem);
+}
+__global__ __launch_bounds__(256, 4) void g2_sk(P pp){
+    __shared__ __align__(16) float smem[4352];
+    g2_task(pp, blockIdx.x, threadIdx.x, smem);
+}
+__global__ __launch_bounds__(256) void a2_sk(P pp){
+    __shared__ __align__(16) float smem[1296];
+    a2_task(pp, blockIdx.x, threadIdx.x, smem);
 }
 
 extern "C" void kernel_launch(void* const* d_in, const int* in_sizes, int n_in,
                               void* d_out, int out_size, void* d_ws, size_t ws_size,
                               hipStream_t stream)
 {
-    const float* feature  = (const float*)d_in[0];
-    const float* adj      = (const float*)d_in[1];
-    const float* main_W1  = (const float*)d_in[2];
-    const float* main_a1s = (const float*)d_in[3];
-    const float* main_a1d = (const float*)d_in[4];
-    const float* main_W2  = (const float*)d_in[5];
-    const float* main_a2s = (const float*)d_in[6];
-    const float* main_a2d = (const float*)d_in[7];
-    const float* dep_W1   = (const float*)d_in[8];
-    const float* dep_a1s  = (const float*)d_in[9];
-    const float* dep_a1d  = (const float*)d_in[10];
-    const float* dep_W2   = (const float*)d_in[11];
-    const float* dep_a2s  = (const float*)d_in[12];
-    const float* dep_a2d  = (const float*)d_in[13];
-    const float* router_W = (const float*)d_in[14];
-    const float* blend_W  = (const float*)d_in[15];
-    const float* blend_b  = (const float*)d_in[16];
-    const int*   doc_p    = (const int*)d_in[17];
-    const int*   sect_p   = (const int*)d_in[18];
+    P hp;
+    hp.feature  = (const float*)d_in[0];
+    hp.adj      = (const float*)d_in[1];
+    hp.main_W1  = (const float*)d_in[2];
+    hp.main_a1s = (const float*)d_in[3];
+    hp.main_a1d = (const float*)d_in[4];
+    hp.main_W2  = (const float*)d_in[5];
+    hp.main_a2s = (const float*)d_in[6];
+    hp.main_a2d = (const float*)d_in[7];
+    hp.dep_W1   = (const float*)d_in[8];
+    hp.dep_a1s  = (const float*)d_in[9];
+    hp.dep_a1d  = (const float*)d_in[10];
+    hp.dep_W2   = (const float*)d_in[11];
+    hp.dep_a2s  = (const float*)d_in[12];
+    hp.dep_a2d  = (const float*)d_in[13];
+    hp.router_W = (const float*)d_in[14];
+    hp.blend_W  = (const float*)d_in[15];
+    hp.blend_b  = (const float*)d_in[16];
+    hp.doc_p    = (const int*)d_in[17];
+    hp.sect_p   = (const int*)d_in[18];
 
     char* ws = (char*)d_ws;
     size_t off = 0;
-    unsigned short* featbf = (unsigned short*)(ws + off); off += (size_t)ROWS*D*2;
-    short*          nbr    = (short*)(ws + off);          off += (size_t)ROWS*MAXN*2;
-    int4*           nbc    = (int4*)(ws + off);           off += (size_t)ROWS*16;
-    unsigned short* w1nk   = (unsigned short*)(ws + off); off += (size_t)4*HHD*D*2;
-    unsigned short* w2nk   = (unsigned short*)(ws + off); off += (size_t)4*D*HHD*2;
-    unsigned short* bwt    = (unsigned short*)(ws + off); off += (size_t)D*D*2;
-    float* es8 = (float*)(ws + off); off += (size_t)4*B*S*8*4;
-    float* ed8 = (float*)(ws + off); off += (size_t)4*B*S*8*4;
-    float* gatebuf = (float*)(ws + off); off += (size_t)ROWS*D*4;
-    unsigned short* htn4 = (unsigned short*)(ws + off); off += (size_t)4*ROWS*HHD*2;
-    unsigned short* h2n4 = (unsigned short*)(ws + off); off += (size_t)4*ROWS*D*2;
-    unsigned short* h1c4 = (unsigned short*)(ws + off); off += (size_t)4*ROWS*HHD*2;
-    float* f2s4    = (float*)(ws + off); off += (size_t)4*ROWS*4;
-    float* f2d4    = (float*)(ws + off); off += (size_t)4*ROWS*4;
-    float* meanV1p = (float*)(ws + off); off += (size_t)4*B*512*4;
-    float* meanV2  = (float*)(ws + off); off += (size_t)4*B*D*4;
-    float* sumBuf  = (float*)(ws + off); off += 128;
-    float* rmask   = (float*)(ws + off); off += (size_t)NE*ROWS*4;
-    float* outp    = (float*)d_out;
-
-    prep_misc_kernel<<<PB_TOTAL, 256, 0, stream>>>(
-        feature, adj, main_W1, dep_W1, main_W2, dep_W2, blend_W, router_W,
-        doc_p, sect_p, featbf, nbr, nbc, w1nk, w2nk, bwt, f2s4, rmask);
-
-    gemm1_kernel<<<dim3(3, ROWS/64, 5), 256, 0, stream>>>(w1nk, featbf, rmask,
-        main_a1s, main_a1d, dep_a1s, dep_a1d, bwt, blend_b,
-        htn4, es8, ed8, meanV1p, gatebuf, sumBuf);
-    attn1_gather_kernel<<<dim3(S, 16), 128, 0, stream>>>(htn4, es8, ed8, nbr, nbc,
-        meanV1p, h1c4);
-    gemm2_kernel<<<dim3(D/128, ROWS/64, 4), 256, 0, stream>>>(w2nk, h1c4,
-        main_a2s, main_a2d, dep_a2s, dep_a2d, h2n4, f2s4, f2d4, meanV2);
-    attn2_blend_kernel<<<dim3(S, B), 256, 0, stream>>>(h2n4, f2s4, f2d4, nbr, nbc,
-        meanV2, gatebuf, rmask, sumBuf, outp);
-}
+    hp.featbf = (unsigned short*)(ws + off); off += (size_t)ROWS*D*2;
+    hp.nbr    = (short*)(ws + off);          off += (size_t)ROWS*MAXN*2;
+    hp.nbc    = (int4*)(ws + off);           off += (size_t)ROWS*16;
+    hp.w1nk   = (unsigned short*)(ws + off); off += (size_t)4*HHD*D*2;
+    hp.w2nk   = (unsigned short*)(ws + off); off += (size_t)4*D*HHD*2;
+    hp.bwt    = (unsigned short*)(ws + off); off += (size_t)D*D*2;
+    hp.es8 = (float*)(ws + off); off += (size_t)4*B*S*8*4;
+    hp.ed8 = (float*)(ws + off); off += (size_t)4*B*S*8*4;
+    hp.gatebuf = (float*)(ws + off); off += (size_t)ROWS*D*4;
+    hp.htn4 = (unsigned short*)(ws + off); off += (size_t)4*ROWS*HHD*2;
+    hp.h2n4 = (unsigned short*)(ws + off); off += (size_t)4*ROWS*D*2;
+    hp.h1c4 = (unsigned short*)(ws + off); off += (size_t)4*ROWS*HHD*2;
+    hp.f2s4    = (float*)(ws + off); off += (size_t)4*ROWS*4;
+    hp.f2d4    = (float*)(ws + off); off += (size_t)4*ROWS*4;
+    hp.meanV1p = (float*)(ws + off); off += (size_t)4*B*512*4;
+    hp.meanV2  = (float*)(ws + off); off += (size_t)4*B*D*4;
+    hp.sumBuf  = (float*)(ws + off); off += 128;
+    hp.rmask   = (float*)(ws + off); off += (size_t)NE*ROWS*4;
+    hp.outp    = (float*)d_out;
+
+    void* args[] = { (void*)&hp };
+    hipError_t err = hipLaunchCooperativeKernel((void*)fused_kernel,
+                                                dim3(NBLK), dim3(256),
+                                                args, 0, stream);
+    if (err != hipSuccess){
+        prep_sk<<<PB_TOTAL, 256, 0, stream>>>(hp);
+        g1_sk<<<896,   256, 0, stream>>>(hp);
+        a1_sk<<<16384, 256, 0, stream>>>(hp);
+        g2_sk<<<512,   256, 0, stream>>>(hp);
+        a2_sk<<<4096,  256, 0, stream>>>(hp);
+    }
+}
```

Measured after the change: 820.8 us. +286.6%, slower.
